# Optimization experiments

Measured on AMD Instinct MI355X. Metric: run time of the kernel, lower is better.

Reference implementation:

```python
import jax, jax.numpy as jnp
import numpy as np

B, C, DE, DE1 = 64, 80, 300, 1024
J, S = 4000, 100            # JOINT_EMB_SIZE, pooling_stride
K = J // S                  # out_in_tmp = 40
FDIM = 2048                 # IMAGE_CHANNEL / CLASSIFIER_CHANNEL


def setup_inputs() -> dict:
    key = jax.random.key(0)
    ks = jax.random.split(key, 14)
    sc = 0.02
    return {
        "feature": jax.random.normal(ks[0], (B, FDIM, 14, 14), jnp.float32),
        "inp": jax.random.normal(ks[1], (C, DE), jnp.float32),
        # A-branch 1x1 convs (Conv2d(300,1024,k=1) == linear over channel dim)
        "Wb1": jax.random.normal(ks[2], (DE1, DE), jnp.float32) * sc,
        "bb1": jnp.zeros((DE1,), jnp.float32),
        "Wb2": jax.random.normal(ks[3], (DE1, DE), jnp.float32) * sc,
        "bb2": jnp.zeros((DE1,), jnp.float32),
        # GCN weights (uniform(-1/sqrt(out), ..) as in reset_parameters)
        "Wg1": jax.random.uniform(ks[4], (DE, 1024), jnp.float32, -1/np.sqrt(1024), 1/np.sqrt(1024)),
        "Wg2": jax.random.uniform(ks[5], (1024, FDIM), jnp.float32, -1/np.sqrt(FDIM), 1/np.sqrt(FDIM)),
        # MFB projections
        "Wimg": jax.random.normal(ks[6], (J, FDIM), jnp.float32) * sc,
        "bimg": jnp.zeros((J,), jnp.float32),
        "Wcls": jax.random.normal(ks[7], (J, FDIM), jnp.float32) * sc,
        "bcls": jnp.zeros((J,), jnp.float32),
        # ML_fc_layer: Linear(C*K, C)
        "Wml": jax.random.normal(ks[8], (C, C * K), jnp.float32) * sc,
        "bml": jnp.zeros((C,), jnp.float32),
    }


def _forward(feature, inp, Wb1, bb1, Wb2, bb2, Wg1, Wg2, Wimg, bimg, Wcls, bcls, Wml, bml):
    # backbone output -> MaxPool2d(14,14) -> [B, 2048]
    feat = jnp.max(feature, axis=(2, 3))
    # inp.view(1, d_e, num_classes, 1): raw row-major reshape (NOT transpose)
    X = inp.reshape(DE, C)                               # [300, 80]
    b1 = jax.nn.sigmoid(Wb1 @ X + bb1[:, None])          # [1024, 80]
    b2 = jax.nn.sigmoid(Wb2 @ X + bb2[:, None])
    A = (b1.T @ b2) / float(C)                           # [80, 80]
    I = jnp.eye(C, dtype=A.dtype)
    A_wave = A + I
    d = A_wave.sum(axis=1) ** -0.5
    d = jnp.where(jnp.isfinite(d), d, 0.0)
    A_hat = d[:, None] * A_wave * d[None, :]             # D^-1/2 A~ D^-1/2
    L_A_loss = jnp.abs(A_hat - I).sum()
    # GCN layers
    h = jax.nn.leaky_relu(A_hat @ (inp @ Wg1), 0.2)      # [80, 1024]
    x = A_hat @ (h @ Wg2)                                # [80, 2048]
    # MFB bilinear pooling, fully batched (dropout off / eval mode)
    img = feat @ Wimg.T + bimg                           # [B, J]
    cls = x @ Wcls.T + bcls                              # [C, J]
    pooled = jnp.einsum('bks,cks->bck', img.reshape(B, K, S), cls.reshape(C, K, S))
    out = pooled.reshape(B, C * K) @ Wml.T + bml         # [B, C]
    return out, L_A_loss


def reference(feature, inp, Wb1, bb1, Wb2, bb2, Wg1, Wg2, Wimg, bimg, Wcls, bcls, Wml, bml):
    return _forward(feature, inp, Wb1, bb1, Wb2, bb2, Wg1, Wg2, Wimg, bimg, Wcls, bcls, Wml, bml)
```

## Files before the change

kernel.cpp:

```cpp
#include <hip/hip_runtime.h>
#include <math.h>

#define B_    64
#define C_    80
#define DE_   300
#define DE1_  1024
#define J_    4000
#define S_    100
#define KP_   40
#define FDIM_ 2048

#define WS_FEAT   0
#define WS_B1     131072
#define WS_B2     212992
#define WS_AW     294912
#define WS_AHAT   301312
#define WS_T1     307712
#define WS_H      389632
#define WS_HH     471552
#define WS_X      553472
#define WS_IMG    717312
#define WS_CLS    973312
#define WS_POOL   1293312

typedef __bf16 bf16x8 __attribute__((ext_vector_type(8)));
typedef float  f32x4  __attribute__((ext_vector_type(4)));

__device__ __forceinline__ bf16x8 cvt_bf16x8(float4 a, float4 b) {
    bf16x8 r;
    r[0] = (__bf16)a.x; r[1] = (__bf16)a.y; r[2] = (__bf16)a.z; r[3] = (__bf16)a.w;
    r[4] = (__bf16)b.x; r[5] = (__bf16)b.y; r[6] = (__bf16)b.z; r[7] = (__bf16)b.w;
    return r;
}

template<int KSTEPS>
__device__ __forceinline__ void mfma_bt_pipe(const float* __restrict__ A0,
                                             const float* __restrict__ B0,
                                             const float* __restrict__ B1,
                                             f32x4& acc0, f32x4& acc1) {
    constexpr int D = 4;
    float4 ra[D][2], rb0[D][2], rb1[D][2];
    #pragma unroll
    for (int p = 0; p < D; ++p) {
        ra[p][0]  = ((const float4*)(A0 + p * 32))[0];
        ra[p][1]  = ((const float4*)(A0 + p * 32))[1];
        rb0[p][0] = ((const float4*)(B0 + p * 32))[0];
        rb0[p][1] = ((const float4*)(B0 + p * 32))[1];
        rb1[p][0] = ((const float4*)(B1 + p * 32))[0];
        rb1[p][1] = ((const float4*)(B1 + p * 32))[1];
    }
    #pragma unroll
    for (int ks = 0; ks < KSTEPS; ++ks) {
        const int slot = ks % D;
        bf16x8 af  = cvt_bf16x8(ra[slot][0],  ra[slot][1]);
        bf16x8 bf0 = cvt_bf16x8(rb0[slot][0], rb0[slot][1]);
        bf16x8 bf1 = cvt_bf16x8(rb1[slot][0], rb1[slot][1]);
        if (ks + D < KSTEPS) {
            ra[slot][0]  = ((const float4*)(A0 + (ks + D) * 32))[0];
            ra[slot][1]  = ((const float4*)(A0 + (ks + D) * 32))[1];
            rb0[slot][0] = ((const float4*)(B0 + (ks + D) * 32))[0];
            rb0[slot][1] = ((const float4*)(B0 + (ks + D) * 32))[1];
            rb1[slot][0] = ((const float4*)(B1 + (ks + D) * 32))[0];
            rb1[slot][1] = ((const float4*)(B1 + (ks + D) * 32))[1];
        }
        acc0 = __builtin_amdgcn_mfma_f32_16x16x32_bf16(af, bf0, acc0, 0, 0, 0);
        acc1 = __builtin_amdgcn_mfma_f32_16x16x32_bf16(af, bf1, acc1, 0, 0, 0);
    }
}

__device__ __forceinline__ void mfma_store_atomic(float* __restrict__ C, int Nst,
                                                  int m0, int n0, int r, int q,
                                                  const f32x4& acc0, const f32x4& acc1) {
    #pragma unroll
    for (int i = 0; i < 4; ++i) {
        int row = m0 + q * 4 + i;
        atomicAdd(&C[(size_t)row * Nst + n0 + r], acc0[i]);
        atomicAdd(&C[(size_t)row * Nst + n0 + 16 + r], acc1[i]);
    }
}

__global__ void fused_init_maxpool(const float* __restrict__ feature,
                                   float* __restrict__ feat,
                                   float* __restrict__ x, float* __restrict__ Aw,
                                   float* __restrict__ t1,
                                   const float* __restrict__ bimg, float* __restrict__ img,
                                   const float* __restrict__ bcls, float* __restrict__ cls) {
    if (blockIdx.x < 32768) {
        int gtid = blockIdx.x * 256 + threadIdx.x;
        int wid  = gtid >> 6;
        int lane = gtid & 63;
        const float* src = feature + (size_t)wid * 196;
        float v = -INFINITY;
        if (lane < 49) {
            float4 u = ((const float4*)src)[lane];
            v = fmaxf(fmaxf(u.x, u.y), fmaxf(u.z, u.w));
        }
        #pragma unroll
        for (int off = 32; off > 0; off >>= 1)
            v = fmaxf(v, __shfl_down(v, off));
        if (lane == 0) feat[wid] = v;
        return;
    }
    int idx = (blockIdx.x - 32768) * 256 + threadIdx.x;
    if (idx < 163840) { x[idx] = 0.0f; return; }
    idx -= 163840;
    if (idx < 6400) {
        int i = idx / 80, j = idx % 80;
        Aw[idx] = (i == j) ? 1.0f : 0.0f;
        return;
    }
    idx -= 6400;
    if (idx < 81920) { t1[idx] = 0.0f; return; }
    idx -= 81920;
    if (idx < 256000) { img[idx] = bimg[idx % 4000]; return; }
    idx -= 256000;
    if (idx < 320000) { cls[idx] = bcls[idx % 4000]; }
}

__global__ void fused_stage2(const float* __restrict__ inp,
                             const float* __restrict__ Wb1, const float* __restrict__ bb1,
                             const float* __restrict__ Wb2, const float* __restrict__ bb2,
                             float* __restrict__ b1, float* __restrict__ b2,
                             const float* __restrict__ Wg1, float* __restrict__ t1) {
    int bid = blockIdx.x;
    if (bid < 640) {
        int idx = bid * 256 + threadIdx.x;
        int which = idx >= 81920;
        int r = which ? idx - 81920 : idx;
        int o = r / 80, c = r % 80;
        const float* W = which ? Wb2 : Wb1;
        const float* bb = which ? bb2 : bb1;
        float acc = bb[o];
        const float* wrow = W + o * 300;
        #pragma unroll 10
        for (int k = 0; k < 300; ++k)
            acc = fmaf(wrow[k], inp[k * 80 + c], acc);
        float s = 1.0f / (1.0f + expf(-acc));
        (which ? b2 : b1)[r] = s;
        return;
    }
    int bid2 = bid - 640;
    int chunk = bid2 / 320, blk = bid2 % 320;
    int idx = blk * 256 + threadIdx.x;
    int m = idx >> 10, n = idx & 1023;
    float acc = 0.f;
    const float* arow = inp + m * 300;
    int k0 = chunk * 75;
    #pragma unroll 5
    for (int k = k0; k < k0 + 75; ++k)
        acc = fmaf(arow[k], Wg1[k * 1024 + n], acc);
    atomicAdd(&t1[idx], acc);
}

__global__ void fused_stage3(const float* __restrict__ b1, const float* __restrict__ b2,
                             float* __restrict__ Aw,
                             const float* __restrict__ feat, const float* __restrict__ Wimg,
                             float* __restrict__ img) {
    int bid = blockIdx.x;
    if (bid < 200) {
        int idx = (bid % 25) * 256 + threadIdx.x;
        int i = idx / 80, j = idx % 80;
        int k0 = (bid / 25) * 128;
        float acc = 0.f;
        #pragma unroll 8
        for (int k = k0; k < k0 + 128; ++k)
            acc = fmaf(b1[k * 80 + i], b2[k * 80 + j], acc);
        atomicAdd(&Aw[idx], acc * (1.0f / 80.0f));
        return;
    }
    int bid3 = bid - 200;
    int nt = bid3 % 125, kc = bid3 / 125;
    int w = threadIdx.x >> 6;
    int lane = threadIdx.x & 63;
    int r = lane & 15, q = lane >> 4;
    int n0 = nt * 32, m0 = w * 16, k0 = kc * 256;
    const float* A0 = feat + (size_t)(m0 + r) * 2048 + k0 + q * 8;
    const float* B0 = Wimg + (size_t)(n0 + r) * 2048 + k0 + q * 8;
    const float* B1 = Wimg + (size_t)(n0 + 16 + r) * 2048 + k0 + q * 8;
    f32x4 acc0 = {0.f, 0.f, 0.f, 0.f}, acc1 = {0.f, 0.f, 0.f, 0.f};
    mfma_bt_pipe<8>(A0, B0, B1, acc0, acc1);
    mfma_store_atomic(img, 4000, m0, n0, r, q, acc0, acc1);
}

__global__ void ahat_kernel(const float* __restrict__ Aw,
                            float* __restrict__ Ahat,
                            float* __restrict__ loss_out) {
    __shared__ float rs[80];
    __shared__ float dsh[80];
    __shared__ float red[256];
    int tid = threadIdx.x;
    if (tid < 80) rs[tid] = 0.f;
    __syncthreads();
    for (int idx = tid; idx < 6400; idx += 256)
        atomicAdd(&rs[idx / 80], Aw[idx]);
    __syncthreads();
    if (tid < 80) {
        float dv = rsqrtf(rs[tid]);
        if (!isfinite(dv)) dv = 0.f;
        dsh[tid] = dv;
    }
    __syncthreads();
    float loss = 0.f;
    for (int idx = tid; idx < 6400; idx += 256) {
        int i = idx / 80, j = idx % 80;
        float ah = dsh[i] * Aw[idx] * dsh[j];
        Ahat[idx] = ah;
        loss += fabsf(ah - (i == j ? 1.0f : 0.0f));
    }
    red[tid] = loss;
    __syncthreads();
    for (int s = 128; s > 0; s >>= 1) {
        if (tid < s) red[tid] += red[tid + s];
        __syncthreads();
    }
    if (tid == 0) *loss_out = red[0];
}

__global__ void h_kernel(const float* __restrict__ Ahat,
                         const float* __restrict__ t1,
                         float* __restrict__ h) {
    int idx = blockIdx.x * 256 + threadIdx.x;
    int m = idx >> 10, n = idx & 1023;
    float acc = 0.f;
    const float* arow = Ahat + m * 80;
    #pragma unroll 8
    for (int k = 0; k < 80; ++k)
        acc = fmaf(arow[k], t1[k * 1024 + n], acc);
    h[idx] = acc > 0.f ? acc : 0.2f * acc;
}

__global__ void hh_kernel(const float* __restrict__ Ahat,
                          const float* __restrict__ h,
                          float* __restrict__ hh) {
    int idx = blockIdx.x * 256 + threadIdx.x;
    int m = idx >> 10, n = idx & 1023;
    float acc = 0.f;
    const float* arow = Ahat + m * 80;
    #pragma unroll 8
    for (int k = 0; k < 80; ++k)
        acc = fmaf(arow[k], h[k * 1024 + n], acc);
    hh[idx] = acc;
}

__global__ __launch_bounds__(320) void gemm_x_mfma(const float* __restrict__ hh,
                                                   const float* __restrict__ Wg2,
                                                   float* __restrict__ x) {
    int w = threadIdx.x >> 6;
    int lane = threadIdx.x & 63;
    int r = lane & 15, q = lane >> 4;
    int n0 = blockIdx.x * 32;
    int k0 = blockIdx.y * 256;
    int m0 = w * 16;

    const float* arow = hh + (size_t)(m0 + r) * 1024 + k0 + q * 8;
    const float* bcol = Wg2 + (size_t)(k0 + q * 8) * 2048 + n0 + r;

    constexpr int D = 4, KS = 8;
    float4 ra[D][2];
    float rb0[D][8], rb1[D][8];
    #pragma unroll
    for (int p = 0; p < D; ++p) {
        ra[p][0] = ((const float4*)(arow + p * 32))[0];
        ra[p][1] = ((const float4*)(arow + p * 32))[1];
        const float* bp = bcol + (size_t)p * 32 * 2048;
        #pragma unroll
        for (int j = 0; j < 8; ++j) {
            rb0[p][j] = bp[(size_t)j * 2048];
            rb1[p][j] = bp[(size_t)j * 2048 + 16];
        }
    }
    f32x4 acc0 = {0.f, 0.f, 0.f, 0.f}, acc1 = {0.f, 0.f, 0.f, 0.f};
    #pragma unroll
    for (int ks = 0; ks < KS; ++ks) {
        const int slot = ks % D;
        bf16x8 af = cvt_bf16x8(ra[slot][0], ra[slot][1]);
        bf16x8 bf0, bf1;
        #pragma unroll
        for (int j = 0; j < 8; ++j) {
            bf0[j] = (__bf16)rb0[slot][j];
            bf1[j] = (__bf16)rb1[slot][j];
        }
        if (ks + D < KS) {
            ra[slot][0] = ((const float4*)(arow + (ks + D) * 32))[0];
            ra[slot][1] = ((const float4*)(arow + (ks + D) * 32))[1];
            const float* bp = bcol + (size_t)(ks + D) * 32 * 2048;
            #pragma unroll
            for (int j = 0; j < 8; ++j) {
                rb0[slot][j] = bp[(size_t)j * 2048];
                rb1[slot][j] = bp[(size_t)j * 2048 + 16];
            }
        }
        acc0 = __builtin_amdgcn_mfma_f32_16x16x32_bf16(af, bf0, acc0, 0, 0, 0);
        acc1 = __builtin_amdgcn_mfma_f32_16x16x32_bf16(af, bf1, acc1, 0, 0, 0);
    }
    mfma_store_atomic(x, 2048, m0, n0, r, q, acc0, acc1);
}

__global__ __launch_bounds__(320) void gemm_cls_mfma(const float* __restrict__ x,
                                                     const float* __restrict__ Wcls,
                                                     float* __restrict__ cls) {
    int w = threadIdx.x >> 6;
    int lane = threadIdx.x & 63;
    int r = lane & 15, q = lane >> 4;
    int n0 = blockIdx.x * 32;
    int k0 = blockIdx.y * 256;
    int m0 = w * 16;
    const float* A0 = x    + (size_t)(m0 + r) * 2048 + k0 + q * 8;
    const float* B0 = Wcls + (size_t)(n0 + r) * 2048 + k0 + q * 8;
    const float* B1 = Wcls + (size_t)(n0 + 16 + r) * 2048 + k0 + q * 8;
    f32x4 acc0 = {0.f, 0.f, 0.f, 0.f}, acc1 = {0.f, 0.f, 0.f, 0.f};
    mfma_bt_pipe<8>(A0, B0, B1, acc0, acc1);
    mfma_store_atomic(cls, 4000, m0, n0, r, q, acc0, acc1);
}

__global__ void pool_kernel(const float* __restrict__ img,
                            const float* __restrict__ cls,
                            float* __restrict__ pooled) {
    int idx = blockIdx.x * 256 + threadIdx.x;
    int b = idx / 3200;
    int rem = idx % 3200;
    int c = rem / 40, k = rem % 40;
    const float4* ia = (const float4*)(img + (size_t)b * 4000 + k * 100);
    const float4* ca = (const float4*)(cls + (size_t)c * 4000 + k * 100);
    float acc = 0.f;
    #pragma unroll 5
    for (int s = 0; s < 25; ++s) {
        float4 u = ia[s], v = ca[s];
        acc = fmaf(u.x, v.x, acc);
        acc = fmaf(u.y, v.y, acc);
        acc = fmaf(u.z, v.z, acc);
        acc = fmaf(u.w, v.w, acc);
    }
    pooled[(size_t)b * 3200 + c * 40 + k] = acc;
}

__global__ void out_kernel(const float* __restrict__ pooled,
                           const float* __restrict__ Wml,
                           const float* __restrict__ bml,
                           float* __restrict__ out) {
    int gid = blockIdx.x * 256 + threadIdx.x;
    int wid = gid >> 6;
    int lane = gid & 63;
    int b = wid / 80, co = wid % 80;
    const float* pr = pooled + (size_t)b * 3200;
    const float* wr = Wml + (size_t)co * 3200;
    float acc = 0.f;
    #pragma unroll 5
    for (int k = lane; k < 3200; k += 64)
        acc = fmaf(pr[k], wr[k], acc);
    #pragma unroll
    for (int off = 32; off > 0; off >>= 1)
        acc += __shfl_down(acc, off);
    if (lane == 0) out[wid] = acc + bml[co];
}

extern "C" void kernel_launch(void* const* d_in, const int* in_sizes, int n_in,
                              void* d_out, int out_size, void* d_ws, size_t ws_size,
                              hipStream_t stream) {
    const float* feature = (const float*)d_in[0];
    const float* inp     = (const float*)d_in[1];
    const float* Wb1     = (const float*)d_in[2];
    const float* bb1     = (const float*)d_in[3];
    const float* Wb2     = (const float*)d_in[4];
    const float* bb2     = (const float*)d_in[5];
    const float* Wg1     = (const float*)d_in[6];
    const float* Wg2     = (const float*)d_in[7];
    const float* Wimg    = (const float*)d_in[8];
    const float* bimg    = (const float*)d_in[9];
    const float* Wcls    = (const float*)d_in[10];
    const float* bcls    = (const float*)d_in[11];
    const float* Wml     = (const float*)d_in[12];
    const float* bml     = (const float*)d_in[13];

    float* ws  = (float*)d_ws;
    float* out = (float*)d_out;

    float* feat   = ws + WS_FEAT;
    float* b1     = ws + WS_B1;
    float* b2     = ws + WS_B2;
    float* Aw     = ws + WS_AW;
    float* Ahat   = ws + WS_AHAT;
    float* t1     = ws + WS_T1;
    float* h      = ws + WS_H;
    float* hh     = ws + WS_HH;
    float* x      = ws + WS_X;
    float* img    = ws + WS_IMG;
    float* cls    = ws + WS_CLS;
    float* pooled = ws + WS_POOL;

    fused_init_maxpool<<<36003, 256, 0, stream>>>(feature, feat, x, Aw, t1,
                                                  bimg, img, bcls, cls);
    fused_stage2<<<1920, 256, 0, stream>>>(inp, Wb1, bb1, Wb2, bb2, b1, b2, Wg1, t1);
    fused_stage3<<<1200, 256, 0, stream>>>(b1, b2, Aw, feat, Wimg, img);
    ahat_kernel<<<1, 256, 0, stream>>>(Aw, Ahat, out + 5120);
    h_kernel<<<320, 256, 0, stream>>>(Ahat, t1, h);
    hh_kernel<<<320, 256, 0, stream>>>(Ahat, h, hh);
    gemm_x_mfma<<<dim3(64, 4), 320, 0, stream>>>(hh, Wg2, x);
    gemm_cls_mfma<<<dim3(125, 8), 320, 0, stream>>>(x, Wcls, cls);
    pool_kernel<<<800, 256, 0, stream>>>(img, cls, pooled);
    out_kernel<<<1280, 256, 0, stream>>>(pooled, Wml, bml, out);
}
```

Before: 346.2 us.

## Merge init/maxpool/stage2 into one kernel and drop the single-block A_hat kernel

Merges the init/maxpool kernel and the b1/b2/t1 stage into one launch. t1 is now computed with a full-K loop and a plain store, so it no longer needs zero-init and atomics. The single-block ahat kernel is removed: each h/hh block recomputes the degree vector and its A_hat row from Aw in shared memory, and the loss is computed by one extra block of the pool kernel. This cuts kernel launches and a serial one-block stage, at the cost of redundant degree computation in every h/hh block.

```diff
diff --git a/kernel.cpp b/kernel.cpp
--- a/kernel.cpp
+++ b/kernel.cpp
@@ -14,7 +14,6 @@
 #define WS_B1     131072
 #define WS_B2     212992
 #define WS_AW     294912
-#define WS_AHAT   301312
 #define WS_T1     307712
 #define WS_H      389632
 #define WS_HH     471552
@@ -79,52 +78,36 @@
     }
 }
 
-__global__ void fused_init_maxpool(const float* __restrict__ feature,
-                                   float* __restrict__ feat,
-                                   float* __restrict__ x, float* __restrict__ Aw,
-                                   float* __restrict__ t1,
-                                   const float* __restrict__ bimg, float* __restrict__ img,
-                                   const float* __restrict__ bcls, float* __restrict__ cls) {
-    if (blockIdx.x < 32768) {
-        int gtid = blockIdx.x * 256 + threadIdx.x;
-        int wid  = gtid >> 6;
-        int lane = gtid & 63;
-        const float* src = feature + (size_t)wid * 196;
-        float v = -INFINITY;
-        if (lane < 49) {
-            float4 u = ((const float4*)src)[lane];
-            v = fmaxf(fmaxf(u.x, u.y), fmaxf(u.z, u.w));
-        }
-        #pragma unroll
-        for (int off = 32; off > 0; off >>= 1)
-            v = fmaxf(v, __shfl_down(v, off));
-        if (lane == 0) feat[wid] = v;
-        return;
-    }
-    int idx = (blockIdx.x - 32768) * 256 + threadIdx.x;
-    if (idx < 163840) { x[idx] = 0.0f; return; }
-    idx -= 163840;
-    if (idx < 6400) {
-        int i = idx / 80, j = idx % 80;
-        Aw[idx] = (i == j) ? 1.0f : 0.0f;
-        return;
-    }
-    idx -= 6400;
-    if (idx < 81920) { t1[idx] = 0.0f; return; }
-    idx -= 81920;
-    if (idx < 256000) { img[idx] = bimg[idx % 4000]; return; }
-    idx -= 256000;
-    if (idx < 320000) { cls[idx] = bcls[idx % 4000]; }
-}
-
-__global__ void fused_stage2(const float* __restrict__ inp,
-                             const float* __restrict__ Wb1, const float* __restrict__ bb1,
-                             const float* __restrict__ Wb2, const float* __restrict__ bb2,
-                             float* __restrict__ b1, float* __restrict__ b2,
-                             const float* __restrict__ Wg1, float* __restrict__ t1) {
+__device__ __forceinline__ void compute_d(const float* __restrict__ Aw,
+                                          float* __restrict__ rs,
+                                          float* __restrict__ dsh, int tid) {
+    if (tid < 80) rs[tid] = 0.f;
+    __syncthreads();
+    #pragma unroll
+    for (int i2 = tid; i2 < 6400; i2 += 256)
+        atomicAdd(&rs[i2 / 80], Aw[i2]);
+    __syncthreads();
+    if (tid < 80) {
+        float dv = rsqrtf(rs[tid]);
+        if (!isfinite(dv)) dv = 0.f;
+        dsh[tid] = dv;
+    }
+    __syncthreads();
+}
+
+__global__ void mega1(const float* __restrict__ feature, float* __restrict__ feat,
+                      const float* __restrict__ inp,
+                      const float* __restrict__ Wb1, const float* __restrict__ bb1,
+                      const float* __restrict__ Wb2, const float* __restrict__ bb2,
+                      float* __restrict__ b1, float* __restrict__ b2,
+                      const float* __restrict__ Wg1, float* __restrict__ t1,
+                      float* __restrict__ x, float* __restrict__ Aw,
+                      const float* __restrict__ bimg, float* __restrict__ img,
+                      const float* __restrict__ bcls, float* __restrict__ cls) {
     int bid = blockIdx.x;
+    int tid = threadIdx.x;
     if (bid < 640) {
-        int idx = bid * 256 + threadIdx.x;
+        int idx = bid * 256 + tid;
         int which = idx >= 81920;
         int r = which ? idx - 81920 : idx;
         int o = r / 80, c = r % 80;
@@ -135,27 +118,54 @@
         #pragma unroll 10
         for (int k = 0; k < 300; ++k)
             acc = fmaf(wrow[k], inp[k * 80 + c], acc);
-        float s = 1.0f / (1.0f + expf(-acc));
-        (which ? b2 : b1)[r] = s;
+        (which ? b2 : b1)[r] = 1.0f / (1.0f + expf(-acc));
         return;
     }
-    int bid2 = bid - 640;
-    int chunk = bid2 / 320, blk = bid2 % 320;
-    int idx = blk * 256 + threadIdx.x;
-    int m = idx >> 10, n = idx & 1023;
-    float acc = 0.f;
-    const float* arow = inp + m * 300;
-    int k0 = chunk * 75;
-    #pragma unroll 5
-    for (int k = k0; k < k0 + 75; ++k)
-        acc = fmaf(arow[k], Wg1[k * 1024 + n], acc);
-    atomicAdd(&t1[idx], acc);
-}
-
-__global__ void fused_stage3(const float* __restrict__ b1, const float* __restrict__ b2,
-                             float* __restrict__ Aw,
-                             const float* __restrict__ feat, const float* __restrict__ Wimg,
-                             float* __restrict__ img) {
+    if (bid < 960) {
+        int idx = (bid - 640) * 256 + tid;
+        int m = idx >> 10, n = idx & 1023;
+        float acc = 0.f;
+        const float* arow = inp + m * 300;
+        #pragma unroll 10
+        for (int k = 0; k < 300; ++k)
+            acc = fmaf(arow[k], Wg1[k * 1024 + n], acc);
+        t1[idx] = acc;
+        return;
+    }
+    if (bid < 3875) {
+        int idx = (bid - 960) * 256 + tid;
+        if (idx < 6400) {
+            int i = idx / 80, j = idx % 80;
+            Aw[idx] = (i == j) ? 1.0f : 0.0f;
+            return;
+        }
+        idx -= 6400;
+        if (idx < 163840) { x[idx] = 0.0f; return; }
+        idx -= 163840;
+        if (idx < 256000) { img[idx] = bimg[idx % 4000]; return; }
+        idx -= 256000;
+        if (idx < 320000) { cls[idx] = bcls[idx % 4000]; }
+        return;
+    }
+    int gtid = (bid - 3875) * 256 + tid;
+    int wid  = gtid >> 6;
+    int lane = gtid & 63;
+    const float* src = feature + (size_t)wid * 196;
+    float v = -INFINITY;
+    if (lane < 49) {
+        float4 u = ((const float4*)src)[lane];
+        v = fmaxf(fmaxf(u.x, u.y), fmaxf(u.z, u.w));
+    }
+    #pragma unroll
+    for (int off = 32; off > 0; off >>= 1)
+        v = fmaxf(v, __shfl_down(v, off));
+    if (lane == 0) feat[wid] = v;
+}
+
+__global__ void mega2(const float* __restrict__ b1, const float* __restrict__ b2,
+                      float* __restrict__ Aw,
+                      const float* __restrict__ feat, const float* __restrict__ Wimg,
+                      float* __restrict__ img) {
     int bid = blockIdx.x;
     if (bid < 200) {
         int idx = (bid % 25) * 256 + threadIdx.x;
@@ -182,64 +192,38 @@
     mfma_store_atomic(img, 4000, m0, n0, r, q, acc0, acc1);
 }
 
-__global__ void ahat_kernel(const float* __restrict__ Aw,
-                            float* __restrict__ Ahat,
-                            float* __restrict__ loss_out) {
-    __shared__ float rs[80];
-    __shared__ float dsh[80];
-    __shared__ float red[256];
-    int tid = threadIdx.x;
-    if (tid < 80) rs[tid] = 0.f;
-    __syncthreads();
-    for (int idx = tid; idx < 6400; idx += 256)
-        atomicAdd(&rs[idx / 80], Aw[idx]);
-    __syncthreads();
-    if (tid < 80) {
-        float dv = rsqrtf(rs[tid]);
-        if (!isfinite(dv)) dv = 0.f;
-        dsh[tid] = dv;
-    }
-    __syncthreads();
-    float loss = 0.f;
-    for (int idx = tid; idx < 6400; idx += 256) {
-        int i = idx / 80, j = idx % 80;
-        float ah = dsh[i] * Aw[idx] * dsh[j];
-        Ahat[idx] = ah;
-        loss += fabsf(ah - (i == j ? 1.0f : 0.0f));
-    }
-    red[tid] = loss;
-    __syncthreads();
-    for (int s = 128; s > 0; s >>= 1) {
-        if (tid < s) red[tid] += red[tid + s];
-        __syncthreads();
-    }
-    if (tid == 0) *loss_out = red[0];
-}
-
-__global__ void h_kernel(const float* __restrict__ Ahat,
+__global__ void h_kernel(const float* __restrict__ Aw,
                          const float* __restrict__ t1,
                          float* __restrict__ h) {
-    int idx = blockIdx.x * 256 + threadIdx.x;
-    int m = idx >> 10, n = idx & 1023;
+    __shared__ float rs[80], dsh[80], ar[80];
+    int tid = threadIdx.x;
+    int m = blockIdx.x >> 2;
+    int n = ((blockIdx.x & 3) << 8) + tid;
+    compute_d(Aw, rs, dsh, tid);
+    if (tid < 80) ar[tid] = dsh[m] * dsh[tid] * Aw[m * 80 + tid];
+    __syncthreads();
     float acc = 0.f;
-    const float* arow = Ahat + m * 80;
     #pragma unroll 8
     for (int k = 0; k < 80; ++k)
-        acc = fmaf(arow[k], t1[k * 1024 + n], acc);
-    h[idx] = acc > 0.f ? acc : 0.2f * acc;
-}
-
-__global__ void hh_kernel(const float* __restrict__ Ahat,
+        acc = fmaf(ar[k], t1[k * 1024 + n], acc);
+    h[(size_t)m * 1024 + n] = acc > 0.f ? acc : 0.2f * acc;
+}
+
+__global__ void hh_kernel(const float* __restrict__ Aw,
                           const float* __restrict__ h,
                           float* __restrict__ hh) {
-    int idx = blockIdx.x * 256 + threadIdx.x;
-    int m = idx >> 10, n = idx & 1023;
+    __shared__ float rs[80], dsh[80], ar[80];
+    int tid = threadIdx.x;
+    int m = blockIdx.x >> 2;
+    int n = ((blockIdx.x & 3) << 8) + tid;
+    compute_d(Aw, rs, dsh, tid);
+    if (tid < 80) ar[tid] = dsh[m] * dsh[tid] * Aw[m * 80 + tid];
+    __syncthreads();
     float acc = 0.f;
-    const float* arow = Ahat + m * 80;
     #pragma unroll 8
     for (int k = 0; k < 80; ++k)
-        acc = fmaf(arow[k], h[k * 1024 + n], acc);
-    hh[idx] = acc;
+        acc = fmaf(ar[k], h[k * 1024 + n], acc);
+    hh[(size_t)m * 1024 + n] = acc;
 }
 
 __global__ __launch_bounds__(320) void gemm_x_mfma(const float* __restrict__ hh,
@@ -313,10 +297,32 @@
     mfma_store_atomic(cls, 4000, m0, n0, r, q, acc0, acc1);
 }
 
-__global__ void pool_kernel(const float* __restrict__ img,
-                            const float* __restrict__ cls,
-                            float* __restrict__ pooled) {
-    int idx = blockIdx.x * 256 + threadIdx.x;
+__global__ void pool_loss_kernel(const float* __restrict__ img,
+                                 const float* __restrict__ cls,
+                                 float* __restrict__ pooled,
+                                 const float* __restrict__ Aw,
+                                 float* __restrict__ loss_out) {
+    int tid = threadIdx.x;
+    if (blockIdx.x == 800) {
+        __shared__ float rs[80], dsh[80];
+        __shared__ float red[256];
+        compute_d(Aw, rs, dsh, tid);
+        float loss = 0.f;
+        for (int idx = tid; idx < 6400; idx += 256) {
+            int i = idx / 80, j = idx % 80;
+            float ah = dsh[i] * Aw[idx] * dsh[j];
+            loss += fabsf(ah - (i == j ? 1.0f : 0.0f));
+        }
+        red[tid] = loss;
+        __syncthreads();
+        for (int s = 128; s > 0; s >>= 1) {
+            if (tid < s) red[tid] += red[tid + s];
+            __syncthreads();
+        }
+        if (tid == 0) *loss_out = red[0];
+        return;
+    }
+    int idx = blockIdx.x * 256 + tid;
     int b = idx / 3200;
     int rem = idx % 3200;
     int c = rem / 40, k = rem % 40;
@@ -379,7 +385,6 @@
     float* b1     = ws + WS_B1;
     float* b2     = ws + WS_B2;
     float* Aw     = ws + WS_AW;
-    float* Ahat   = ws + WS_AHAT;
     float* t1     = ws + WS_T1;
     float* h      = ws + WS_H;
     float* hh     = ws + WS_HH;
@@ -388,15 +393,13 @@
     float* cls    = ws + WS_CLS;
     float* pooled = ws + WS_POOL;
 
-    fused_init_maxpool<<<36003, 256, 0, stream>>>(feature, feat, x, Aw, t1,
-                                                  bimg, img, bcls, cls);
-    fused_stage2<<<1920, 256, 0, stream>>>(inp, Wb1, bb1, Wb2, bb2, b1, b2, Wg1, t1);
-    fused_stage3<<<1200, 256, 0, stream>>>(b1, b2, Aw, feat, Wimg, img);
-    ahat_kernel<<<1, 256, 0, stream>>>(Aw, Ahat, out + 5120);
-    h_kernel<<<320, 256, 0, stream>>>(Ahat, t1, h);
-    hh_kernel<<<320, 256, 0, stream>>>(Ahat, h, hh);
+    mega1<<<36643, 256, 0, stream>>>(feature, feat, inp, Wb1, bb1, Wb2, bb2,
+                                     b1, b2, Wg1, t1, x, Aw, bimg, img, bcls, cls);
+    mega2<<<1200, 256, 0, stream>>>(b1, b2, Aw, feat, Wimg, img);
+    h_kernel<<<320, 256, 0, stream>>>(Aw, t1, h);
+    hh_kernel<<<320, 256, 0, stream>>>(Aw, h, hh);
     gemm_x_mfma<<<dim3(64, 4), 320, 0, stream>>>(hh, Wg2, x);
     gemm_cls_mfma<<<dim3(125, 8), 320, 0, stream>>>(x, Wcls, cls);
-    pool_kernel<<<800, 256, 0, stream>>>(img, cls, pooled);
+    pool_loss_kernel<<<801, 256, 0, stream>>>(img, cls, pooled, Aw, out + 5120);
     out_kernel<<<1280, 256, 0, stream>>>(pooled, Wml, bml, out);
 }
```

Result: slower. 365.6 us (+5.6%).
